# Kernel tuning notes

Hardware: AMD Instinct MI355X
Metric: run time of the kernel (lower is better)

The kernel has to match this reference:

```python
import jax, jax.numpy as jnp
import numpy as np
import math

B, S, HID = 2, 1024, 2048
N_HEAD, N_KV = 16, 4
HEAD = HID // N_HEAD          # 128
N_REP = N_HEAD // N_KV        # 4


def setup_inputs() -> dict:
    key = jax.random.key(0)
    ks = jax.random.split(key, 5)
    x = jax.random.normal(ks[0], (B, S, HID), dtype=jnp.float32)
    # realistic RoPE tables: freqs over half dim, duplicated (rotate_half convention)
    inv_freq = 1.0 / (10000.0 ** (np.arange(0, HEAD, 2, dtype=np.float32) / HEAD))
    t = np.arange(S, dtype=np.float32)
    freqs = np.outer(t, inv_freq)                    # [S, HEAD/2]
    emb = np.concatenate([freqs, freqs], axis=-1)    # [S, HEAD]
    cos = jnp.asarray(np.cos(emb), dtype=jnp.float32)
    sin = jnp.asarray(np.sin(emb), dtype=jnp.float32)
    sc = 0.02
    wq = jax.random.normal(ks[1], (HID, HID), dtype=jnp.float32) * sc
    wk = jax.random.normal(ks[2], (HID, N_KV * HEAD), dtype=jnp.float32) * sc
    wv = jax.random.normal(ks[3], (HID, N_KV * HEAD), dtype=jnp.float32) * sc
    wo = jax.random.normal(ks[4], (HID, HID), dtype=jnp.float32) * sc
    return {"x": x, "cos": cos, "sin": sin, "wq": wq, "wk": wk, "wv": wv, "wo": wo}


def _rotate_half(t):
    h = t.shape[-1] // 2
    return jnp.concatenate([-t[..., h:], t[..., :h]], axis=-1)


def reference(x, cos, sin, wq, wk, wv, wo):
    b, s, _ = x.shape
    q = (x @ wq).reshape(b, s, N_HEAD, HEAD)   # [B,S,H,D]
    k = (x @ wk).reshape(b, s, N_KV, HEAD)     # [B,S,Kv,D]
    v = (x @ wv).reshape(b, s, N_KV, HEAD)
    # RoPE: cos/sin [S,D] -> [S,1,D], broadcasts over batch and heads
    c = cos[:s, None, :]
    sn = sin[:s, None, :]
    q = q * c + _rotate_half(q) * sn
    k = k * c + _rotate_half(k) * sn
    # GQA: repeat kv heads to match query heads
    k = jnp.repeat(k, N_REP, axis=2)           # [B,S,H,D]
    v = jnp.repeat(v, N_REP, axis=2)
    q = q.transpose(0, 2, 1, 3)                # [B,H,S,D]
    k = k.transpose(0, 2, 1, 3)
    v = v.transpose(0, 2, 1, 3)
    scores = jnp.einsum("bhqd,bhkd->bhqk", q, k) / math.sqrt(HEAD)
    causal = jnp.triu(jnp.full((s, s), -jnp.inf, dtype=scores.dtype), k=1)
    scores = scores + causal[None, None, :, :]
    probs = jax.nn.softmax(scores.astype(jnp.float32), axis=-1).astype(q.dtype)
    out = jnp.einsum("bhqk,bhkd->bhqd", probs, v)   # [B,H,S,D]
    out = out.transpose(0, 2, 1, 3).reshape(b, s, N_HEAD * HEAD)
    return out @ wo
```

## Files before the change

### kernel.cpp

```cpp
#include <hip/hip_runtime.h>
#include <hip/hip_bf16.h>
#include <math.h>
#include <stdint.h>

#define BATCH 2
#define SEQ   1024
#define HID   2048
#define NH    16
#define NKV   4
#define HEAD  128
#define MROWS (BATCH*SEQ)
#define QSC   0.08838834764831845f

typedef _Float16 f16;
typedef _Float16 f16x8 __attribute__((ext_vector_type(8)));
typedef __fp16   h16x2 __attribute__((ext_vector_type(2)));
typedef float    f32x4 __attribute__((ext_vector_type(4)));

__device__ __forceinline__ void glds16(const void* g, void* l) {
    __builtin_amdgcn_global_load_lds(
        (const __attribute__((address_space(1))) void*)g,
        (__attribute__((address_space(3))) void*)l, 16, 0, 0);
}

__device__ __forceinline__ f32x4 mfma16(f16x8 a, f16x8 b, f32x4 c) {
    return __builtin_amdgcn_mfma_f32_16x16x32_f16(a, b, c, 0, 0, 0);
}

__global__ __launch_bounds__(256)
void cvt_f32_f16(const float* __restrict__ in, f16* __restrict__ out) {
    int i = blockIdx.x * 256 + threadIdx.x;
    float4 v = ((const float4*)in)[i];
    union { ushort4 u; f16 h[4]; } o;
    o.h[0] = (f16)v.x; o.h[1] = (f16)v.y; o.h[2] = (f16)v.z; o.h[3] = (f16)v.w;
    ((ushort4*)out)[i] = o.u;
}

__global__ __launch_bounds__(256)
void transW(const float* __restrict__ w0, const float* __restrict__ w1,
            const float* __restrict__ w2, f16* __restrict__ out,
            int c1, int c2, int ld0, int ld1, int ld2) {
    __shared__ float t[64][65];
    const int n0 = blockIdx.x * 64, k0 = blockIdx.y * 64;
    const float* W; int ld, cb;
    if (n0 < c1)      { W = w0; ld = ld0; cb = 0;  }
    else if (n0 < c2) { W = w1; ld = ld1; cb = c1; }
    else              { W = w2; ld = ld2; cb = c2; }
    const int tr = threadIdx.x >> 4, tc = threadIdx.x & 15;
    #pragma unroll
    for (int i = 0; i < 4; ++i) {
        int row = tr * 4 + i;
        float4 v = *(const float4*)&W[(size_t)(k0 + row) * ld + (n0 - cb) + tc * 4];
        t[row][tc*4+0] = v.x; t[row][tc*4+1] = v.y;
        t[row][tc*4+2] = v.z; t[row][tc*4+3] = v.w;
    }
    __syncthreads();
    #pragma unroll
    for (int i = 0; i < 4; ++i) {
        int nrow = tr * 4 + i;
        union { ushort4 u; f16 h[4]; } o;
        o.h[0] = (f16)t[tc*4+0][nrow]; o.h[1] = (f16)t[tc*4+1][nrow];
        o.h[2] = (f16)t[tc*4+2][nrow]; o.h[3] = (f16)t[tc*4+3][nrow];
        *(ushort4*)&out[(size_t)(n0 + nrow) * 2048 + k0 + tc * 4] = o.u;
    }
}

template<int MODE>
__global__ __launch_bounds__(256)
void gemm16(const f16* __restrict__ A, const f16* __restrict__ Bt,
            f16* __restrict__ Oq, f16* __restrict__ Ok, f16* __restrict__ Ov,
            float* __restrict__ Of, int ntn)
{
    __shared__ f16 As[128 * 64];
    __shared__ f16 Bs[64 * 64];
    const int tid   = threadIdx.x;
    const int lane  = tid & 63;
    const int wid   = tid >> 6;
    const int col_l = lane & 15;
    const int hi    = lane >> 4;

    const int nwg = gridDim.x;
    const int cpx = nwg >> 3;
    const int bid = blockIdx.x;
    const int sw  = (bid & 7) * cpx + (bid >> 3);
    const int n0  = (sw % ntn) * 64;
    const int m0  = (sw / ntn) * 128;

    f32x4 acc[2][4];
    #pragma unroll
    for (int mt = 0; mt < 2; ++mt)
        #pragma unroll
        for (int nt = 0; nt < 4; ++nt)
            acc[mt][nt] = (f32x4){0.f, 0.f, 0.f, 0.f};

    #pragma unroll 1
    for (int kt = 0; kt < 32; ++kt) {
        #pragma unroll
        for (int j = 0; j < 4; ++j) {
            int gidx = j * 256 + tid;
            int r = gidx >> 3, g = gidx & 7;
            int gs = (g ^ (r & 7)) << 3;
            glds16(A + (size_t)(m0 + r) * 2048 + kt * 64 + gs,
                   (char*)As + (size_t)(j * 256 + (wid << 6)) * 16);
        }
        #pragma unroll
        for (int j = 0; j < 2; ++j) {
            int gidx = j * 256 + tid;
            int r = gidx >> 3, g = gidx & 7;
            int gs = (g ^ (r & 7)) << 3;
            glds16(Bt + (size_t)(n0 + r) * 2048 + kt * 64 + gs,
                   (char*)Bs + (size_t)(j * 256 + (wid << 6)) * 16);
        }
        asm volatile("s_waitcnt vmcnt(0)" ::: "memory");
        __syncthreads();

        #pragma unroll
        for (int ks = 0; ks < 2; ++ks) {
            int gr = (ks << 2) | hi;
            int ar0 = wid * 32 + col_l;
            int ar1 = ar0 + 16;
            f16x8 a0 = *(const f16x8*)&As[ar0 * 64 + ((gr ^ (ar0 & 7)) << 3)];
            f16x8 a1 = *(const f16x8*)&As[ar1 * 64 + ((gr ^ (ar1 & 7)) << 3)];
            #pragma unroll
            for (int nt = 0; nt < 4; ++nt) {
                int br = nt * 16 + col_l;
                f16x8 b = *(const f16x8*)&Bs[br * 64 + ((gr ^ (br & 7)) << 3)];
                acc[0][nt] = mfma16(a0, b, acc[0][nt]);
                acc[1][nt] = mfma16(a1, b, acc[1][nt]);
            }
        }
        __syncthreads();
    }

    if (MODE == 0) {
        #pragma unroll
        for (int mt = 0; mt < 2; ++mt)
            #pragma unroll
            for (int r = 0; r < 4; ++r) {
                int grow = m0 + wid * 32 + mt * 16 + hi * 4 + r;
                #pragma unroll
                for (int nt = 0; nt < 4; ++nt)
                    Of[(size_t)grow * 2048 + n0 + nt * 16 + col_l] = acc[mt][nt][r];
            }
    } else if (n0 < 2048) {
        #pragma unroll
        for (int mt = 0; mt < 2; ++mt)
            #pragma unroll
            for (int r = 0; r < 4; ++r) {
                int grow = m0 + wid * 32 + mt * 16 + hi * 4 + r;
                #pragma unroll
                for (int nt = 0; nt < 4; ++nt)
                    Oq[(size_t)grow * 2048 + n0 + nt * 16 + col_l] = (f16)acc[mt][nt][r];
            }
    } else if (n0 < 2560) {
        #pragma unroll
        for (int mt = 0; mt < 2; ++mt)
            #pragma unroll
            for (int r = 0; r < 4; ++r) {
                int grow = m0 + wid * 32 + mt * 16 + hi * 4 + r;
                #pragma unroll
                for (int nt = 0; nt < 4; ++nt)
                    Ok[(size_t)grow * 512 + (n0 - 2048) + nt * 16 + col_l] = (f16)acc[mt][nt][r];
            }
    } else {
        #pragma unroll
        for (int mt = 0; mt < 2; ++mt) {
            int grow0 = m0 + wid * 32 + mt * 16 + hi * 4;
            int bb = grow0 >> 10, s0 = grow0 & (SEQ - 1);
            #pragma unroll
            for (int nt = 0; nt < 4; ++nt) {
                int vcol = (n0 - 2560) + nt * 16 + col_l;
                int kvh = vcol >> 7, d = vcol & 127;
                union { ushort4 u; f16 h[4]; } pv;
                #pragma unroll
                for (int r = 0; r < 4; ++r) pv.h[r] = (f16)acc[mt][nt][r];
                *(ushort4*)&Ov[(size_t)((bb * 4 + kvh) * 128 + d) * 1024 + s0] = pv.u;
            }
        }
    }
}

__global__ __launch_bounds__(256)
void rope_qk(f16* __restrict__ q16, f16* __restrict__ k16,
             const float* __restrict__ cosp, const float* __restrict__ sinp)
{
    int t = blockIdx.x * 256 + threadIdx.x;
    f16* p; int row, head, quad; float sc;
    if (t < 2048 * 256) {
        row = t >> 8; int rem = t & 255; head = rem >> 4; quad = rem & 15;
        p = q16 + (size_t)row * 2048 + head * 128 + quad * 4;
        sc = QSC;
    } else {
        int u = t - 2048 * 256;
        row = u >> 6; int rem = u & 63; head = rem >> 4; quad = rem & 15;
        p = k16 + (size_t)row * 512 + head * 128 + quad * 4;
        sc = 1.f;
    }
    const int srow = row & (SEQ - 1);
    const int d0 = quad * 4;
    float4 c4 = *(const float4*)&cosp[srow * HEAD + d0];
    float4 s4 = *(const float4*)&sinp[srow * HEAD + d0];
    union { ushort4 u; f16 h[4]; } lo, hv, olo, ohi;
    lo.u = *(ushort4*)p;
    hv.u = *(ushort4*)(p + 64);
    const float c[4] = {c4.x, c4.y, c4.z, c4.w};
    const float s[4] = {s4.x, s4.y, s4.z, s4.w};
    #pragma unroll
    for (int e = 0; e < 4; ++e) {
        float fl = (float)lo.h[e], fh = (float)hv.h[e];
        olo.h[e] = (f16)((fl * c[e] - fh * s[e]) * sc);
        ohi.h[e] = (f16)((fh * c[e] + fl * s[e]) * sc);
    }
    *(ushort4*)p        = olo.u;
    *(ushort4*)(p + 64) = ohi.u;
}

__global__ __launch_bounds__(256, 2)
void attn16(const f16* __restrict__ q16, const f16* __restrict__ k16,
            const f16* __restrict__ vT, f16* __restrict__ attnb)
{
    __shared__ f16 Ks[2][32 * 128];
    __shared__ f16 Vs[2][128 * 32];

    const int tid   = threadIdx.x;
    const int lane  = tid & 63;
    const int wid   = tid >> 6;
    const int col_l = lane & 15;
    const int hi    = lane >> 4;

    const int bx = blockIdx.x;
    const int qt = (bx < 256) ? (15 - (bx >> 5)) : ((bx - 256) >> 5);
    const int bh = bx & 31;
    const int b  = bh >> 4;
    const int h  = bh & 15;
    const int kv = h >> 2;
    const int qrow = qt * 64 + wid * 16 + col_l;

    f16x8 qf[4];
    {
        const f16* qp = q16 + (size_t)(b * SEQ + qrow) * 2048 + h * 128 + hi * 8;
        #pragma unroll
        for (int ks = 0; ks < 4; ++ks) qf[ks] = *(const f16x8*)&qp[ks * 32];
    }
    const f16* vTg = vT + (size_t)(b * 4 + kv) * 128 * 1024;

    auto stage = [&](int buf, int kt) {
        #pragma unroll
        for (int j = 0; j < 2; ++j) {
            int gidx = j * 256 + tid;
            int r = gidx >> 4, g = gidx & 15;
            glds16(k16 + (size_t)(b * SEQ + kt * 32 + r) * 512 + kv * 128 + ((g ^ (r & 7)) << 3),
                   (char*)&Ks[buf][0] + (size_t)(j * 256 + (wid << 6)) * 16);
            int d = gidx >> 2, g2 = gidx & 3;
            glds16(vTg + (size_t)d * 1024 + kt * 32 + ((g2 ^ (d & 3)) << 3),
                   (char*)&Vs[buf][0] + (size_t)(j * 256 + (wid << 6)) * 16);
        }
    };

    f32x4 O[8];
    #pragma unroll
    for (int dt = 0; dt < 8; ++dt) O[dt] = (f32x4){0.f, 0.f, 0.f, 0.f};
    float mrun = -INFINITY, lrun = 0.f;

    const int ntiles = 2 * (qt + 1);
    stage(0, 0);
    asm volatile("s_waitcnt vmcnt(0)" ::: "memory");
    __syncthreads();

    int cur = 0;
    #pragma unroll 1
    for (int kt = 0; kt < ntiles; ++kt) {
        if (kt + 1 < ntiles) stage(cur ^ 1, kt + 1);

        f32x4 S0 = (f32x4){0.f,0.f,0.f,0.f}, S1 = (f32x4){0.f,0.f,0.f,0.f};
        #pragma unroll
        for (int ks = 0; ks < 4; ++ks) {
            int gr = (ks << 2) | hi;
            int r0 = col_l, r1 = col_l + 16;
            f16x8 kf0 = *(const f16x8*)&Ks[cur][r0 * 128 + ((gr ^ (r0 & 7)) << 3)];
            f16x8 kf1 = *(const f16x8*)&Ks[cur][r1 * 128 + ((gr ^ (r1 & 7)) << 3)];
            S0 = mfma16(kf0, qf[ks], S0);
            S1 = mfma16(kf1, qf[ks], S1);
        }
        float p[8];
        p[0]=S0[0]; p[1]=S0[1]; p[2]=S0[2]; p[3]=S0[3];
        p[4]=S1[0]; p[5]=S1[1]; p[6]=S1[2]; p[7]=S1[3];

        #pragma unroll
        for (int sl = 0; sl < 8; ++sl) {
            int kk = kt * 32 + (sl >> 2) * 16 + hi * 4 + (sl & 3);
            if (kk > qrow) p[sl] = -INFINITY;
        }

        float mt = p[0];
        #pragma unroll
        for (int sl = 1; sl < 8; ++sl) mt = fmaxf(mt, p[sl]);
        mt = fmaxf(mt, __shfl_xor(mt, 16));
        mt = fmaxf(mt, __shfl_xor(mt, 32));
        float mnew = fmaxf(mrun, mt);
        float corr = __expf(mrun - mnew);
        mrun = mnew;
        float ps = 0.f;
        #pragma unroll
        for (int sl = 0; sl < 8; ++sl) { p[sl] = __expf(p[sl] - mnew); ps += p[sl]; }
        ps += __shfl_xor(ps, 16);
        ps += __shfl_xor(ps, 32);
        lrun = lrun * corr + ps;

        union U2 { h16x2 h; int i; };
        int pk[4];
        { U2 u; u.h = __builtin_amdgcn_cvt_pkrtz(p[0], p[1]); pk[0] = u.i; }
        { U2 u; u.h = __builtin_amdgcn_cvt_pkrtz(p[2], p[3]); pk[1] = u.i; }
        { U2 u; u.h = __builtin_amdgcn_cvt_pkrtz(p[4], p[5]); pk[2] = u.i; }
        { U2 u; u.h = __builtin_amdgcn_cvt_pkrtz(p[6], p[7]); pk[3] = u.i; }
        union UA { f16x8 v; int i[4]; } ua;
        #pragma unroll
        for (int j = 0; j < 4; ++j) {
            int srcl = col_l + 16 * ((2 * hi + (j >> 1)) & 3);
            int v0 = __builtin_amdgcn_ds_bpermute(srcl << 2, pk[j & 1]);
            int v1 = __builtin_amdgcn_ds_bpermute(srcl << 2, pk[(j & 1) + 2]);
            ua.i[j] = (hi >= 2) ? v1 : v0;
        }

        float cb[4];
        #pragma unroll
        for (int r = 0; r < 4; ++r)
            cb[r] = __int_as_float(__builtin_amdgcn_ds_bpermute((hi * 4 + r) << 2,
                                                                __float_as_int(corr)));
        #pragma unroll
        for (int dt = 0; dt < 8; ++dt) {
            O[dt][0] *= cb[0]; O[dt][1] *= cb[1];
            O[dt][2] *= cb[2]; O[dt][3] *= cb[3];
        }

        #pragma unroll
        for (int dt = 0; dt < 8; ++dt) {
            int vr = dt * 16 + col_l;
            f16x8 vf = *(const f16x8*)&Vs[cur][vr * 32 + (((hi) ^ (vr & 3)) << 3)];
            O[dt] = mfma16(ua.v, vf, O[dt]);
        }

        if (kt + 1 < ntiles) {
            asm volatile("s_waitcnt vmcnt(0)" ::: "memory");
            __syncthreads();
            cur ^= 1;
        }
    }

    float linv = 1.f / lrun;
    float lb[4];
    #pragma unroll
    for (int r = 0; r < 4; ++r)
        lb[r] = __int_as_float(__builtin_amdgcn_ds_bpermute((hi * 4 + r) << 2,
                                                            __float_as_int(linv)));
    #pragma unroll
    for (int dt = 0; dt < 8; ++dt)
        #pragma unroll
        for (int r = 0; r < 4; ++r) {
            int row = b * SEQ + qt * 64 + wid * 16 + hi * 4 + r;
            attnb[(size_t)row * 2048 + h * 128 + dt * 16 + col_l] = (f16)(O[dt][r] * lb[r]);
        }
}

extern "C" void kernel_launch(void* const* d_in, const int* in_sizes, int n_in,
                              void* d_out, int out_size, void* d_ws, size_t ws_size,
                              hipStream_t stream)
{
    const float* x    = (const float*)d_in[0];
    const float* cosp = (const float*)d_in[1];
    const float* sinp = (const float*)d_in[2];
    const float* wq   = (const float*)d_in[3];
    const float* wk   = (const float*)d_in[4];
    const float* wv   = (const float*)d_in[5];
    const float* wo   = (const float*)d_in[6];
    float* out = (float*)d_out;

    char* ws = (char*)d_ws;
    f16* x16    = (f16*)(ws);
    f16* attn16v= (f16*)(ws);
    f16* Wqkvt  = (f16*)(ws + 8388608);
    f16* Wot    = (f16*)(ws + 8388608);
    f16* q16    = (f16*)(ws + 20971520);
    f16* k16    = (f16*)(ws + 29360128);
    f16* vT     = (f16*)(ws + 31457280);

    cvt_f32_f16<<<4096, 256, 0, stream>>>(x, x16);

    transW<<<dim3(48, 32), 256, 0, stream>>>(wq, wk, wv, Wqkvt, 2048, 2560, 2048, 512, 512);

    gemm16<1><<<768, 256, 0, stream>>>(x16, Wqkvt, q16, k16, vT, nullptr, 48);

    rope_qk<<<2560, 256, 0, stream>>>(q16, k16, cosp, sinp);

    transW<<<dim3(32, 32), 256, 0, stream>>>(wo, wo, wo, Wot, 2048, 2048, 2048, 2048, 2048);

    attn16<<<512, 256, 0, stream>>>(q16, k16, vT, attn16v);

    gemm16<0><<<512, 256, 0, stream>>>(attn16v, Wot, nullptr, nullptr, nullptr, out, 32);
}
```

Baseline: 220.6 us.

## Merge prep kernels, fuse Q RoPE into attention, widen KV tiles to 64

The input cast and both weight transposes are merged into one prep kernel, with Wo given its own workspace slot so it no longer aliases Wqkvt. Q RoPE and scaling move into the attention kernel's Q load, so the separate RoPE pass now touches only K. The attention kernel now processes 64-key tiles instead of 32, applies the causal mask only on the diagonal tile, and reorders blocks so each head's query tiles are grouped. This removes launches and a full Q read/write pass and halves the loop iterations, at the cost of doubled LDS use per block, which may reduce occupancy.

```diff
diff --git a/kernel.cpp b/kernel.cpp
--- a/kernel.cpp
+++ b/kernel.cpp
@@ -28,29 +28,38 @@
 }
 
 __global__ __launch_bounds__(256)
-void cvt_f32_f16(const float* __restrict__ in, f16* __restrict__ out) {
-    int i = blockIdx.x * 256 + threadIdx.x;
-    float4 v = ((const float4*)in)[i];
-    union { ushort4 u; f16 h[4]; } o;
-    o.h[0] = (f16)v.x; o.h[1] = (f16)v.y; o.h[2] = (f16)v.z; o.h[3] = (f16)v.w;
-    ((ushort4*)out)[i] = o.u;
-}
-
-__global__ __launch_bounds__(256)
-void transW(const float* __restrict__ w0, const float* __restrict__ w1,
-            const float* __restrict__ w2, f16* __restrict__ out,
-            int c1, int c2, int ld0, int ld1, int ld2) {
+void prep(const float* __restrict__ x,
+          const float* __restrict__ wq, const float* __restrict__ wk,
+          const float* __restrict__ wv, const float* __restrict__ wo,
+          f16* __restrict__ x16, f16* __restrict__ Wqkvt, f16* __restrict__ Wot)
+{
     __shared__ float t[64][65];
-    const int n0 = blockIdx.x * 64, k0 = blockIdx.y * 64;
-    const float* W; int ld, cb;
-    if (n0 < c1)      { W = w0; ld = ld0; cb = 0;  }
-    else if (n0 < c2) { W = w1; ld = ld1; cb = c1; }
-    else              { W = w2; ld = ld2; cb = c2; }
-    const int tr = threadIdx.x >> 4, tc = threadIdx.x & 15;
+    const int bid = blockIdx.x, tid = threadIdx.x;
+    if (bid < 4096) {
+        int i = bid * 256 + tid;
+        float4 v = ((const float4*)x)[i];
+        union { ushort4 u; f16 h[4]; } o;
+        o.h[0] = (f16)v.x; o.h[1] = (f16)v.y; o.h[2] = (f16)v.z; o.h[3] = (f16)v.w;
+        ((ushort4*)x16)[i] = o.u;
+        return;
+    }
+    const float* W; int ld, cs, k0, n0; f16* out;
+    if (bid < 5632) {
+        int b2 = bid - 4096;
+        n0 = (b2 % 48) * 64; k0 = (b2 / 48) * 64; out = Wqkvt;
+        if (n0 < 2048)      { W = wq; ld = 2048; cs = n0; }
+        else if (n0 < 2560) { W = wk; ld = 512;  cs = n0 - 2048; }
+        else                { W = wv; ld = 512;  cs = n0 - 2560; }
+    } else {
+        int b3 = bid - 5632;
+        n0 = (b3 % 32) * 64; k0 = (b3 / 32) * 64; out = Wot;
+        W = wo; ld = 2048; cs = n0;
+    }
+    const int tr = tid >> 4, tc = tid & 15;
     #pragma unroll
     for (int i = 0; i < 4; ++i) {
         int row = tr * 4 + i;
-        float4 v = *(const float4*)&W[(size_t)(k0 + row) * ld + (n0 - cb) + tc * 4];
+        float4 v = *(const float4*)&W[(size_t)(k0 + row) * ld + cs + tc * 4];
         t[row][tc*4+0] = v.x; t[row][tc*4+1] = v.y;
         t[row][tc*4+2] = v.z; t[row][tc*4+3] = v.w;
     }
@@ -181,21 +190,12 @@
 }
 
 __global__ __launch_bounds__(256)
-void rope_qk(f16* __restrict__ q16, f16* __restrict__ k16,
-             const float* __restrict__ cosp, const float* __restrict__ sinp)
+void rope_k(f16* __restrict__ k16,
+            const float* __restrict__ cosp, const float* __restrict__ sinp)
 {
     int t = blockIdx.x * 256 + threadIdx.x;
-    f16* p; int row, head, quad; float sc;
-    if (t < 2048 * 256) {
-        row = t >> 8; int rem = t & 255; head = rem >> 4; quad = rem & 15;
-        p = q16 + (size_t)row * 2048 + head * 128 + quad * 4;
-        sc = QSC;
-    } else {
-        int u = t - 2048 * 256;
-        row = u >> 6; int rem = u & 63; head = rem >> 4; quad = rem & 15;
-        p = k16 + (size_t)row * 512 + head * 128 + quad * 4;
-        sc = 1.f;
-    }
+    int row = t >> 6; int rem = t & 63; int head = rem >> 4; int quad = rem & 15;
+    f16* p = k16 + (size_t)row * 512 + head * 128 + quad * 4;
     const int srow = row & (SEQ - 1);
     const int d0 = quad * 4;
     float4 c4 = *(const float4*)&cosp[srow * HEAD + d0];
@@ -208,8 +208,8 @@
     #pragma unroll
     for (int e = 0; e < 4; ++e) {
         float fl = (float)lo.h[e], fh = (float)hv.h[e];
-        olo.h[e] = (f16)((fl * c[e] - fh * s[e]) * sc);
-        ohi.h[e] = (f16)((fh * c[e] + fl * s[e]) * sc);
+        olo.h[e] = (f16)(fl * c[e] - fh * s[e]);
+        ohi.h[e] = (f16)(fh * c[e] + fl * s[e]);
     }
     *(ushort4*)p        = olo.u;
     *(ushort4*)(p + 64) = ohi.u;
@@ -217,10 +217,12 @@
 
 __global__ __launch_bounds__(256, 2)
 void attn16(const f16* __restrict__ q16, const f16* __restrict__ k16,
-            const f16* __restrict__ vT, f16* __restrict__ attnb)
+            const f16* __restrict__ vT,
+            const float* __restrict__ cosp, const float* __restrict__ sinp,
+            f16* __restrict__ attnb)
 {
-    __shared__ f16 Ks[2][32 * 128];
-    __shared__ f16 Vs[2][128 * 32];
+    __shared__ f16 Ks[2][64 * 128];
+    __shared__ f16 Vs[2][128 * 64];
 
     const int tid   = threadIdx.x;
     const int lane  = tid & 63;
@@ -229,8 +231,11 @@
     const int hi    = lane >> 4;
 
     const int bx = blockIdx.x;
-    const int qt = (bx < 256) ? (15 - (bx >> 5)) : ((bx - 256) >> 5);
-    const int bh = bx & 31;
+    const int r8 = bx >> 8;
+    const int c  = bx & 255;
+    const int bh = c >> 3;
+    const int j8 = c & 7;
+    const int qt = r8 ? j8 : (15 - j8);
     const int b  = bh >> 4;
     const int h  = bh & 15;
     const int kv = h >> 2;
@@ -239,20 +244,41 @@
     f16x8 qf[4];
     {
         const f16* qp = q16 + (size_t)(b * SEQ + qrow) * 2048 + h * 128 + hi * 8;
-        #pragma unroll
-        for (int ks = 0; ks < 4; ++ks) qf[ks] = *(const f16x8*)&qp[ks * 32];
+        f16x8 raw[4];
+        #pragma unroll
+        for (int ks = 0; ks < 4; ++ks) raw[ks] = *(const f16x8*)&qp[ks * 32];
+        #pragma unroll
+        for (int ks = 0; ks < 2; ++ks) {
+            union { float4 v; float a[4]; } c0, c1, s0, s1;
+            const float* cp = cosp + qrow * HEAD + ks * 32 + hi * 8;
+            const float* sp = sinp + qrow * HEAD + ks * 32 + hi * 8;
+            c0.v = *(const float4*)cp;  c1.v = *(const float4*)(cp + 4);
+            s0.v = *(const float4*)sp;  s1.v = *(const float4*)(sp + 4);
+            #pragma unroll
+            for (int e = 0; e < 8; ++e) {
+                float cc = (e < 4) ? c0.a[e & 3] : c1.a[e & 3];
+                float sv = (e < 4) ? s0.a[e & 3] : s1.a[e & 3];
+                float lo = (float)raw[ks][e], hv = (float)raw[ks + 2][e];
+                qf[ks][e]     = (f16)((lo * cc - hv * sv) * QSC);
+                qf[ks + 2][e] = (f16)((hv * cc + lo * sv) * QSC);
+            }
+        }
     }
     const f16* vTg = vT + (size_t)(b * 4 + kv) * 128 * 1024;
 
     auto stage = [&](int buf, int kt) {
         #pragma unroll
-        for (int j = 0; j < 2; ++j) {
+        for (int j = 0; j < 4; ++j) {
             int gidx = j * 256 + tid;
             int r = gidx >> 4, g = gidx & 15;
-            glds16(k16 + (size_t)(b * SEQ + kt * 32 + r) * 512 + kv * 128 + ((g ^ (r & 7)) << 3),
+            glds16(k16 + (size_t)(b * SEQ + kt * 64 + r) * 512 + kv * 128 + ((g ^ (r & 7)) << 3),
                    (char*)&Ks[buf][0] + (size_t)(j * 256 + (wid << 6)) * 16);
-            int d = gidx >> 2, g2 = gidx & 3;
-            glds16(vTg + (size_t)d * 1024 + kt * 32 + ((g2 ^ (d & 3)) << 3),
+        }
+        #pragma unroll
+        for (int j = 0; j < 4; ++j) {
+            int gidx = j * 256 + tid;
+            int d = gidx >> 3, g = gidx & 7;
+            glds16(vTg + (size_t)d * 1024 + kt * 64 + ((g ^ (d & 7)) << 3),
                    (char*)&Vs[buf][0] + (size_t)(j * 256 + (wid << 6)) * 16);
         }
     };
@@ -262,7 +288,7 @@
     for (int dt = 0; dt < 8; ++dt) O[dt] = (f32x4){0.f, 0.f, 0.f, 0.f};
     float mrun = -INFINITY, lrun = 0.f;
 
-    const int ntiles = 2 * (qt + 1);
+    const int ntiles = qt + 1;
     stage(0, 0);
     asm volatile("s_waitcnt vmcnt(0)" ::: "memory");
     __syncthreads();
@@ -272,29 +298,37 @@
     for (int kt = 0; kt < ntiles; ++kt) {
         if (kt + 1 < ntiles) stage(cur ^ 1, kt + 1);
 
-        f32x4 S0 = (f32x4){0.f,0.f,0.f,0.f}, S1 = (f32x4){0.f,0.f,0.f,0.f};
+        f32x4 S[4];
+        #pragma unroll
+        for (int t = 0; t < 4; ++t) S[t] = (f32x4){0.f, 0.f, 0.f, 0.f};
         #pragma unroll
         for (int ks = 0; ks < 4; ++ks) {
             int gr = (ks << 2) | hi;
-            int r0 = col_l, r1 = col_l + 16;
-            f16x8 kf0 = *(const f16x8*)&Ks[cur][r0 * 128 + ((gr ^ (r0 & 7)) << 3)];
-            f16x8 kf1 = *(const f16x8*)&Ks[cur][r1 * 128 + ((gr ^ (r1 & 7)) << 3)];
-            S0 = mfma16(kf0, qf[ks], S0);
-            S1 = mfma16(kf1, qf[ks], S1);
-        }
-        float p[8];
-        p[0]=S0[0]; p[1]=S0[1]; p[2]=S0[2]; p[3]=S0[3];
-        p[4]=S1[0]; p[5]=S1[1]; p[6]=S1[2]; p[7]=S1[3];
-
-        #pragma unroll
-        for (int sl = 0; sl < 8; ++sl) {
-            int kk = kt * 32 + (sl >> 2) * 16 + hi * 4 + (sl & 3);
-            if (kk > qrow) p[sl] = -INFINITY;
+            #pragma unroll
+            for (int t = 0; t < 4; ++t) {
+                int rr = t * 16 + col_l;
+                f16x8 kf = *(const f16x8*)&Ks[cur][rr * 128 + ((gr ^ (rr & 7)) << 3)];
+                S[t] = mfma16(kf, qf[ks], S[t]);
+            }
+        }
+        float p[16];
+        #pragma unroll
+        for (int t = 0; t < 4; ++t) {
+            p[t*4+0] = S[t][0]; p[t*4+1] = S[t][1];
+            p[t*4+2] = S[t][2]; p[t*4+3] = S[t][3];
+        }
+
+        if (kt == qt) {
+            #pragma unroll
+            for (int sl = 0; sl < 16; ++sl) {
+                int kk = kt * 64 + (sl >> 2) * 16 + hi * 4 + (sl & 3);
+                if (kk > qrow) p[sl] = -INFINITY;
+            }
         }
 
         float mt = p[0];
         #pragma unroll
-        for (int sl = 1; sl < 8; ++sl) mt = fmaxf(mt, p[sl]);
+        for (int sl = 1; sl < 16; ++sl) mt = fmaxf(mt, p[sl]);
         mt = fmaxf(mt, __shfl_xor(mt, 16));
         mt = fmaxf(mt, __shfl_xor(mt, 32));
         float mnew = fmaxf(mrun, mt);
@@ -302,24 +336,28 @@
         mrun = mnew;
         float ps = 0.f;
         #pragma unroll
-        for (int sl = 0; sl < 8; ++sl) { p[sl] = __expf(p[sl] - mnew); ps += p[sl]; }
+        for (int sl = 0; sl < 16; ++sl) { p[sl] = __expf(p[sl] - mnew); ps += p[sl]; }
         ps += __shfl_xor(ps, 16);
         ps += __shfl_xor(ps, 32);
         lrun = lrun * corr + ps;
 
         union U2 { h16x2 h; int i; };
-        int pk[4];
-        { U2 u; u.h = __builtin_amdgcn_cvt_pkrtz(p[0], p[1]); pk[0] = u.i; }
-        { U2 u; u.h = __builtin_amdgcn_cvt_pkrtz(p[2], p[3]); pk[1] = u.i; }
-        { U2 u; u.h = __builtin_amdgcn_cvt_pkrtz(p[4], p[5]); pk[2] = u.i; }
-        { U2 u; u.h = __builtin_amdgcn_cvt_pkrtz(p[6], p[7]); pk[3] = u.i; }
-        union UA { f16x8 v; int i[4]; } ua;
+        int pk[8];
+        #pragma unroll
+        for (int t = 0; t < 4; ++t) {
+            { U2 u; u.h = __builtin_amdgcn_cvt_pkrtz(p[t*4+0], p[t*4+1]); pk[t*2+0] = u.i; }
+            { U2 u; u.h = __builtin_amdgcn_cvt_pkrtz(p[t*4+2], p[t*4+3]); pk[t*2+1] = u.i; }
+        }
+        union UA { f16x8 v; int i[4]; } F0, F1;
         #pragma unroll
         for (int j = 0; j < 4; ++j) {
             int srcl = col_l + 16 * ((2 * hi + (j >> 1)) & 3);
-            int v0 = __builtin_amdgcn_ds_bpermute(srcl << 2, pk[j & 1]);
-            int v1 = __builtin_amdgcn_ds_bpermute(srcl << 2, pk[(j & 1) + 2]);
-            ua.i[j] = (hi >= 2) ? v1 : v0;
+            int a0 = __builtin_amdgcn_ds_bpermute(srcl << 2, pk[j & 1]);
+            int a1 = __builtin_amdgcn_ds_bpermute(srcl << 2, pk[2 + (j & 1)]);
+            F0.i[j] = (hi >= 2) ? a1 : a0;
+            int b0 = __builtin_amdgcn_ds_bpermute(srcl << 2, pk[4 + (j & 1)]);
+            int b1 = __builtin_amdgcn_ds_bpermute(srcl << 2, pk[6 + (j & 1)]);
+            F1.i[j] = (hi >= 2) ? b1 : b0;
         }
 
         float cb[4];
@@ -336,8 +374,10 @@
         #pragma unroll
         for (int dt = 0; dt < 8; ++dt) {
             int vr = dt * 16 + col_l;
-            f16x8 vf = *(const f16x8*)&Vs[cur][vr * 32 + (((hi) ^ (vr & 3)) << 3)];
-            O[dt] = mfma16(ua.v, vf, O[dt]);
+            f16x8 v0 = *(const f16x8*)&Vs[cur][vr * 64 + ((hi ^ (vr & 7)) << 3)];
+            O[dt] = mfma16(F0.v, v0, O[dt]);
+            f16x8 v1 = *(const f16x8*)&Vs[cur][vr * 64 + (((4 | hi) ^ (vr & 7)) << 3)];
+            O[dt] = mfma16(F1.v, v1, O[dt]);
         }
 
         if (kt + 1 < ntiles) {
@@ -379,22 +419,18 @@
     f16* x16    = (f16*)(ws);
     f16* attn16v= (f16*)(ws);
     f16* Wqkvt  = (f16*)(ws + 8388608);
-    f16* Wot    = (f16*)(ws + 8388608);
     f16* q16    = (f16*)(ws + 20971520);
     f16* k16    = (f16*)(ws + 29360128);
     f16* vT     = (f16*)(ws + 31457280);
-
-    cvt_f32_f16<<<4096, 256, 0, stream>>>(x, x16);
-
-    transW<<<dim3(48, 32), 256, 0, stream>>>(wq, wk, wv, Wqkvt, 2048, 2560, 2048, 512, 512);
+    f16* Wot    = (f16*)(ws + 33554432);
+
+    prep<<<6656, 256, 0, stream>>>(x, wq, wk, wv, wo, x16, Wqkvt, Wot);
 
     gemm16<1><<<768, 256, 0, stream>>>(x16, Wqkvt, q16, k16, vT, nullptr, 48);
 
-    rope_qk<<<2560, 256, 0, stream>>>(q16, k16, cosp, sinp);
-
-    transW<<<dim3(32, 32), 256, 0, stream>>>(wo, wo, wo, Wot, 2048, 2048, 2048, 2048, 2048);
-
-    attn16<<<512, 256, 0, stream>>>(q16, k16, vT, attn16v);
+    rope_k<<<512, 256, 0, stream>>>(k16, cosp, sinp);
+
+    attn16<<<512, 256, 0, stream>>>(q16, k16, vT, cosp, sinp, attn16v);
 
     gemm16<0><<<512, 256, 0, stream>>>(attn16v, Wot, nullptr, nullptr, nullptr, out, 32);
 }
```

Measured after the change: 203.9 us. 1.08x faster.
